# Performance work log

Measured on AMD Instinct MI355X. Metric: run time of the kernel, lower is better.

Reference implementation:

```python
import jax, jax.numpy as jnp
import numpy as np

MARGIN = 0.5
HIERARCHY_LEVEL = 0
EPS = 1e-05


def setup_inputs() -> dict:
    key = jax.random.key(0)
    k1, k2, k3, k4 = jax.random.split(key, 4)
    n, m, d, L, n_classes = 4096, 32768, 128, 2, 100
    embeddings = jax.random.normal(k1, (n, d), dtype=jnp.float32)
    ref_embeddings = jax.random.normal(k2, (m, d), dtype=jnp.float32)
    labels = jax.random.randint(k3, (n, L), 0, n_classes, dtype=jnp.int64)
    ref_labels = jax.random.randint(k4, (m, L), 0, n_classes, dtype=jnp.int64)
    return {"embeddings": embeddings, "labels": labels,
            "ref_embeddings": ref_embeddings, "ref_labels": ref_labels}


def reference(embeddings, labels, ref_embeddings, ref_labels):
    # select hierarchy level
    lab = labels[:, HIERARCHY_LEVEL]          # [n]
    ref_lab = ref_labels[:, HIERARCHY_LEVEL]  # [m]
    n = embeddings.shape[0]
    sim = embeddings @ ref_embeddings.T       # [n, m]
    same = lab[:, None] == ref_lab[None, :]   # [n, m] bool
    # positive pairs: same label and sim < 1 - eps -> contribute (1 - sim)
    pos_mask = same & (sim < 1.0 - EPS)
    # negative pairs: different label and sim > margin -> contribute sim
    neg_mask = (~same) & (sim > MARGIN)
    pos_loss = jnp.sum(jnp.where(pos_mask, 1.0 - sim, 0.0))
    neg_loss = jnp.sum(jnp.where(neg_mask, sim, 0.0))
    return (pos_loss + neg_loss) / n
```

## Files before the change

### kernel.cpp

```cpp
#include <hip/hip_runtime.h>
#include <stdint.h>

#define N_EMB 4096
#define M_REF 32768
#define D_K   128
#define BM    128
#define BN    128
#define NCOLTILES 16
#define COLCHUNK (BN * NCOLTILES)
#define NCCHUNK (M_REF / COLCHUNK)
#define NROWT  (N_EMB / BM)

typedef __attribute__((ext_vector_type(8))) short short8;
typedef __attribute__((ext_vector_type(4))) float float4v;

static __device__ __forceinline__ unsigned short f2bf(float f) {
    unsigned int u = __builtin_bit_cast(unsigned int, f);
    u += 0x7FFFu + ((u >> 16) & 1u);
    return (unsigned short)(u >> 16);
}

__global__ void cvt_kernel(const float* __restrict__ emb, const float* __restrict__ ref,
                           unsigned short* __restrict__ aw, unsigned short* __restrict__ bw) {
    const int NA4 = N_EMB * D_K / 4;
    const int NB4 = M_REF * D_K / 4;
    int stride = gridDim.x * blockDim.x;
    for (int i = blockIdx.x * blockDim.x + threadIdx.x; i < NA4 + NB4; i += stride) {
        const float4* src;
        unsigned short* dst;
        int j;
        if (i < NA4) { src = (const float4*)emb; dst = aw; j = i; }
        else         { src = (const float4*)ref; dst = bw; j = i - NA4; }
        float4 v = src[j];
        ushort4 o;
        o.x = f2bf(v.x); o.y = f2bf(v.y); o.z = f2bf(v.z); o.w = f2bf(v.w);
        *(ushort4*)(dst + (size_t)j * 4) = o;
    }
}

static __device__ __forceinline__ void gld_lds16(const void* g, void* l) {
    __builtin_amdgcn_global_load_lds((__attribute__((address_space(1))) void*)g,
                                     (__attribute__((address_space(3))) void*)l,
                                     16, 0, 0);
}

__launch_bounds__(256, 2)
__global__ void xbm_kernel(const unsigned short* __restrict__ aw,
                           const unsigned short* __restrict__ bw,
                           const int* __restrict__ lab,
                           const int* __restrict__ rlab,
                           float* __restrict__ out) {
    __shared__ unsigned short a_sm[BM * D_K];
    __shared__ unsigned short b_sm[BN * D_K];
    __shared__ float red_sm[4];

    const int tid  = threadIdx.x;
    const int lane = tid & 63;
    const int wave = tid >> 6;
    const int wm = wave >> 1, wn = wave & 1;
    const int quad = lane >> 4;
    const int l15  = lane & 15;

    const int rtile  = blockIdx.x >> 4;
    const int cchunk = blockIdx.x & 15;
    const int row0 = rtile * BM;
    const int col0 = cchunk * COLCHUNK;

    #pragma unroll
    for (int i = 0; i < 8; ++i) {
        int c  = i * 256 + tid;
        int r  = c >> 4;
        int ch = c & 15;
        int sc = ch ^ (r & 15);
        gld_lds16((const char*)aw + ((size_t)(row0 + r) * D_K + sc * 8) * 2,
                  (char*)a_sm + (size_t)c * 16);
    }

    int labv[4][4];
    #pragma unroll
    for (int mt = 0; mt < 4; ++mt)
        #pragma unroll
        for (int r = 0; r < 4; ++r) {
            int row = row0 + wm * 64 + mt * 16 + quad * 4 + r;
            labv[mt][r] = lab[row * 2];
        }

    __syncthreads();

    short8 a_reg[4][4];
    #pragma unroll
    for (int mt = 0; mt < 4; ++mt) {
        int ml = wm * 64 + mt * 16 + l15;
        #pragma unroll
        for (int ks = 0; ks < 4; ++ks) {
            int ch = ks * 4 + quad;
            int cs = ch ^ (ml & 15);
            a_reg[mt][ks] = *(const short8*)(a_sm + (size_t)ml * D_K + cs * 8);
        }
    }

    float loss = 0.0f;

    for (int t = 0; t < NCOLTILES; ++t) {
        const int cbase = col0 + t * BN;

        #pragma unroll
        for (int i = 0; i < 8; ++i) {
            int c  = i * 256 + tid;
            int r  = c >> 4;
            int ch = c & 15;
            int sc = ch ^ (r & 15);
            gld_lds16((const char*)bw + ((size_t)(cbase + r) * D_K + sc * 8) * 2,
                      (char*)b_sm + (size_t)c * 16);
        }
        __syncthreads();

        float4v acc[4][4] = {};
        #pragma unroll
        for (int ks = 0; ks < 4; ++ks) {
            short8 b_reg[4];
            #pragma unroll
            for (int nt = 0; nt < 4; ++nt) {
                int nl = wn * 64 + nt * 16 + l15;
                int ch = ks * 4 + quad;
                int cs = ch ^ (nl & 15);
                b_reg[nt] = *(const short8*)(b_sm + (size_t)nl * D_K + cs * 8);
            }
            #pragma unroll
            for (int mt = 0; mt < 4; ++mt)
                #pragma unroll
                for (int nt = 0; nt < 4; ++nt)
                    acc[mt][nt] = __builtin_amdgcn_mfma_f32_16x16x32_bf16(
                        a_reg[mt][ks], b_reg[nt], acc[mt][nt], 0, 0, 0);
        }
        __syncthreads();

        int rl[4];
        #pragma unroll
        for (int nt = 0; nt < 4; ++nt) {
            int cix = cbase + wn * 64 + nt * 16 + l15;
            rl[nt] = rlab[cix * 2];
        }
        #pragma unroll
        for (int mt = 0; mt < 4; ++mt)
            #pragma unroll
            for (int nt = 0; nt < 4; ++nt)
                #pragma unroll
                for (int r = 0; r < 4; ++r) {
                    float s = acc[mt][nt][r];
                    float pos = fmaxf(1.0f - s, 0.0f);
                    float neg = (s > 0.5f) ? s : 0.0f;
                    loss += (labv[mt][r] == rl[nt]) ? pos : neg;
                }
    }

    #pragma unroll
    for (int off = 32; off > 0; off >>= 1)
        loss += __shfl_down(loss, off, 64);
    if (lane == 0) red_sm[wave] = loss;
    __syncthreads();
    if (tid == 0) {
        float v = (red_sm[0] + red_sm[1] + red_sm[2] + red_sm[3]) * (1.0f / (float)N_EMB);
        atomicAdd(out, v);
    }
}

extern "C" void kernel_launch(void* const* d_in, const int* in_sizes, int n_in,
                              void* d_out, int out_size, void* d_ws, size_t ws_size,
                              hipStream_t stream) {
    const float* emb     = (const float*)d_in[0];
    const int*   labels  = (const int*)d_in[1];
    const float* ref     = (const float*)d_in[2];
    const int*   rlabels = (const int*)d_in[3];
    float* out = (float*)d_out;

    unsigned short* aw = (unsigned short*)d_ws;
    unsigned short* bw = aw + (size_t)N_EMB * D_K;

    hipMemsetAsync(d_out, 0, sizeof(float), stream);
    cvt_kernel<<<512, 256, 0, stream>>>(emb, ref, aw, bw);
    xbm_kernel<<<NROWT * NCCHUNK, 256, 0, stream>>>(aw, bw, labels, rlabels, out);
}
```

Before: 119.0 us.

## Double-buffer B tiles with BN=64, reuse LDS for A, fold memset into convert

Halves the column tile to 64, so the LDS footprint can be reused: the A tile is staged through the two B buffers, then those buffers double-buffer B tiles, prefetching the next tile while MFMAs run on the current one. This removes one barrier per iteration and lets three blocks fit per CU, at the cost of more blocks and more reloads of A per column. The output memset moves into the convert kernel, which now launches twice as many blocks, to save one launch. Loss is accumulated in four partial sums to shorten the dependency chain.

```diff
diff --git a/kernel.cpp b/kernel.cpp
--- a/kernel.cpp
+++ b/kernel.cpp
@@ -5,7 +5,7 @@
 #define M_REF 32768
 #define D_K   128
 #define BM    128
-#define BN    128
+#define BN    64
 #define NCOLTILES 16
 #define COLCHUNK (BN * NCOLTILES)
 #define NCCHUNK (M_REF / COLCHUNK)
@@ -21,7 +21,9 @@
 }
 
 __global__ void cvt_kernel(const float* __restrict__ emb, const float* __restrict__ ref,
-                           unsigned short* __restrict__ aw, unsigned short* __restrict__ bw) {
+                           unsigned short* __restrict__ aw, unsigned short* __restrict__ bw,
+                           float* __restrict__ out) {
+    if (blockIdx.x == 0 && threadIdx.x == 0) out[0] = 0.0f;
     const int NA4 = N_EMB * D_K / 4;
     const int NB4 = M_REF * D_K / 4;
     int stride = gridDim.x * blockDim.x;
@@ -44,14 +46,13 @@
                                      16, 0, 0);
 }
 
-__launch_bounds__(256, 2)
+__launch_bounds__(256, 3)
 __global__ void xbm_kernel(const unsigned short* __restrict__ aw,
                            const unsigned short* __restrict__ bw,
                            const int* __restrict__ lab,
                            const int* __restrict__ rlab,
                            float* __restrict__ out) {
-    __shared__ unsigned short a_sm[BM * D_K];
-    __shared__ unsigned short b_sm[BN * D_K];
+    __shared__ unsigned short sm[2][BN * D_K];
     __shared__ float red_sm[4];
 
     const int tid  = threadIdx.x;
@@ -61,8 +62,8 @@
     const int quad = lane >> 4;
     const int l15  = lane & 15;
 
-    const int rtile  = blockIdx.x >> 4;
-    const int cchunk = blockIdx.x & 15;
+    const int rtile  = blockIdx.x >> 5;
+    const int cchunk = blockIdx.x & 31;
     const int row0 = rtile * BM;
     const int col0 = cchunk * COLCHUNK;
 
@@ -73,7 +74,7 @@
         int ch = c & 15;
         int sc = ch ^ (r & 15);
         gld_lds16((const char*)aw + ((size_t)(row0 + r) * D_K + sc * 8) * 2,
-                  (char*)a_sm + (size_t)c * 16);
+                  (char*)&sm[r >> 6][(r & 63) * D_K + ch * 8]);
     }
 
     int labv[4][4];
@@ -95,64 +96,80 @@
         for (int ks = 0; ks < 4; ++ks) {
             int ch = ks * 4 + quad;
             int cs = ch ^ (ml & 15);
-            a_reg[mt][ks] = *(const short8*)(a_sm + (size_t)ml * D_K + cs * 8);
+            a_reg[mt][ks] = *(const short8*)(&sm[wm][(ml & 63) * D_K + cs * 8]);
         }
     }
 
-    float loss = 0.0f;
+    __syncthreads();
+
+    #pragma unroll
+    for (int i = 0; i < 4; ++i) {
+        int c  = i * 256 + tid;
+        int r  = c >> 4;
+        int ch = c & 15;
+        int sc = ch ^ (r & 15);
+        gld_lds16((const char*)bw + ((size_t)(col0 + r) * D_K + sc * 8) * 2,
+                  (char*)&sm[0][r * D_K + ch * 8]);
+    }
+
+    float lossa[4] = {0.0f, 0.0f, 0.0f, 0.0f};
 
     for (int t = 0; t < NCOLTILES; ++t) {
         const int cbase = col0 + t * BN;
+        const int buf = t & 1;
 
-        #pragma unroll
-        for (int i = 0; i < 8; ++i) {
-            int c  = i * 256 + tid;
-            int r  = c >> 4;
-            int ch = c & 15;
-            int sc = ch ^ (r & 15);
-            gld_lds16((const char*)bw + ((size_t)(cbase + r) * D_K + sc * 8) * 2,
-                      (char*)b_sm + (size_t)c * 16);
-        }
         __syncthreads();
 
-        float4v acc[4][4] = {};
+        if (t + 1 < NCOLTILES) {
+            #pragma unroll
+            for (int i = 0; i < 4; ++i) {
+                int c  = i * 256 + tid;
+                int r  = c >> 4;
+                int ch = c & 15;
+                int sc = ch ^ (r & 15);
+                gld_lds16((const char*)bw + ((size_t)(cbase + BN + r) * D_K + sc * 8) * 2,
+                          (char*)&sm[buf ^ 1][r * D_K + ch * 8]);
+            }
+        }
+
+        int rl[2];
+        #pragma unroll
+        for (int nt = 0; nt < 2; ++nt)
+            rl[nt] = rlab[(cbase + wn * 32 + nt * 16 + l15) * 2];
+
+        float4v acc[4][2] = {};
         #pragma unroll
         for (int ks = 0; ks < 4; ++ks) {
-            short8 b_reg[4];
+            short8 b_reg[2];
             #pragma unroll
-            for (int nt = 0; nt < 4; ++nt) {
-                int nl = wn * 64 + nt * 16 + l15;
+            for (int nt = 0; nt < 2; ++nt) {
+                int nl = wn * 32 + nt * 16 + l15;
                 int ch = ks * 4 + quad;
                 int cs = ch ^ (nl & 15);
-                b_reg[nt] = *(const short8*)(b_sm + (size_t)nl * D_K + cs * 8);
+                b_reg[nt] = *(const short8*)(&sm[buf][nl * D_K + cs * 8]);
             }
             #pragma unroll
             for (int mt = 0; mt < 4; ++mt)
                 #pragma unroll
-                for (int nt = 0; nt < 4; ++nt)
+                for (int nt = 0; nt < 2; ++nt)
                     acc[mt][nt] = __builtin_amdgcn_mfma_f32_16x16x32_bf16(
                         a_reg[mt][ks], b_reg[nt], acc[mt][nt], 0, 0, 0);
         }
-        __syncthreads();
 
-        int rl[4];
-        #pragma unroll
-        for (int nt = 0; nt < 4; ++nt) {
-            int cix = cbase + wn * 64 + nt * 16 + l15;
-            rl[nt] = rlab[cix * 2];
-        }
         #pragma unroll
         for (int mt = 0; mt < 4; ++mt)
             #pragma unroll
-            for (int nt = 0; nt < 4; ++nt)
+            for (int nt = 0; nt < 2; ++nt)
                 #pragma unroll
                 for (int r = 0; r < 4; ++r) {
                     float s = acc[mt][nt][r];
                     float pos = fmaxf(1.0f - s, 0.0f);
                     float neg = (s > 0.5f) ? s : 0.0f;
-                    loss += (labv[mt][r] == rl[nt]) ? pos : neg;
+                    lossa[mt] += (labv[mt][r] == rl[nt]) ? pos : neg;
                 }
     }
+
+    float loss = (lossa[0] + lossa[1]) + (lossa[2] + lossa[3]);
 
     #pragma unroll
     for (int off = 32; off > 0; off >>= 1)
@@ -177,7 +194,6 @@
     unsigned short* aw = (unsigned short*)d_ws;
     unsigned short* bw = aw + (size_t)N_EMB * D_K;
 
-    hipMemsetAsync(d_out, 0, sizeof(float), stream);
-    cvt_kernel<<<512, 256, 0, stream>>>(emb, ref, aw, bw);
+    cvt_kernel<<<1024, 256, 0, stream>>>(emb, ref, aw, bw, out);
     xbm_kernel<<<NROWT * NCCHUNK, 256, 0, stream>>>(aw, bw, labels, rlabels, out);
 }
```

After: 121.5 us. +2.1%, slower.

## Load MFMA operands directly from global, drop LDS staging and memset

Applied to the files above, without the earlier changes.

Removes the LDS staging of A and B tiles and the block barriers; each wave now loads its MFMA fragments straight from global memory, relying on L1/L2 for reuse across waves. The output zeroing moves into the convert kernel in place of a separate memset, the convert grid is doubled, and the loss is split across four accumulators to shorten dependency chains. Without LDS, every wave fetches B through the caches, which raises global traffic and may expose load latency because there is no explicit prefetch.

```diff
diff --git a/kernel.cpp b/kernel.cpp
--- a/kernel.cpp
+++ b/kernel.cpp
@@ -21,7 +21,9 @@
 }
 
 __global__ void cvt_kernel(const float* __restrict__ emb, const float* __restrict__ ref,
-                           unsigned short* __restrict__ aw, unsigned short* __restrict__ bw) {
+                           unsigned short* __restrict__ aw, unsigned short* __restrict__ bw,
+                           float* __restrict__ out) {
+    if (blockIdx.x == 0 && threadIdx.x == 0) out[0] = 0.0f;
     const int NA4 = N_EMB * D_K / 4;
     const int NB4 = M_REF * D_K / 4;
     int stride = gridDim.x * blockDim.x;
@@ -38,20 +40,12 @@
     }
 }
 
-static __device__ __forceinline__ void gld_lds16(const void* g, void* l) {
-    __builtin_amdgcn_global_load_lds((__attribute__((address_space(1))) void*)g,
-                                     (__attribute__((address_space(3))) void*)l,
-                                     16, 0, 0);
-}
-
 __launch_bounds__(256, 2)
 __global__ void xbm_kernel(const unsigned short* __restrict__ aw,
                            const unsigned short* __restrict__ bw,
                            const int* __restrict__ lab,
                            const int* __restrict__ rlab,
                            float* __restrict__ out) {
-    __shared__ unsigned short a_sm[BM * D_K];
-    __shared__ unsigned short b_sm[BN * D_K];
     __shared__ float red_sm[4];
 
     const int tid  = threadIdx.x;
@@ -66,54 +60,32 @@
     const int row0 = rtile * BM;
     const int col0 = cchunk * COLCHUNK;
 
+    short8 a_reg[4][4];
     #pragma unroll
-    for (int i = 0; i < 8; ++i) {
-        int c  = i * 256 + tid;
-        int r  = c >> 4;
-        int ch = c & 15;
-        int sc = ch ^ (r & 15);
-        gld_lds16((const char*)aw + ((size_t)(row0 + r) * D_K + sc * 8) * 2,
-                  (char*)a_sm + (size_t)c * 16);
+    for (int mt = 0; mt < 4; ++mt) {
+        const int row = row0 + wm * 64 + mt * 16 + l15;
+        #pragma unroll
+        for (int ks = 0; ks < 4; ++ks)
+            a_reg[mt][ks] = *(const short8*)(aw + (size_t)row * D_K + ks * 32 + quad * 8);
     }
 
     int labv[4][4];
     #pragma unroll
     for (int mt = 0; mt < 4; ++mt)
         #pragma unroll
-        for (int r = 0; r < 4; ++r) {
-            int row = row0 + wm * 64 + mt * 16 + quad * 4 + r;
-            labv[mt][r] = lab[row * 2];
-        }
+        for (int r = 0; r < 4; ++r)
+            labv[mt][r] = lab[(row0 + wm * 64 + mt * 16 + quad * 4 + r) * 2];
 
-    __syncthreads();
+    float lossa[4] = {0.0f, 0.0f, 0.0f, 0.0f};
 
-    short8 a_reg[4][4];
-    #pragma unroll
-    for (int mt = 0; mt < 4; ++mt) {
-        int ml = wm * 64 + mt * 16 + l15;
-        #pragma unroll
-        for (int ks = 0; ks < 4; ++ks) {
-            int ch = ks * 4 + quad;
-            int cs = ch ^ (ml & 15);
-            a_reg[mt][ks] = *(const short8*)(a_sm + (size_t)ml * D_K + cs * 8);
-        }
-    }
-
-    float loss = 0.0f;
+    const unsigned short* bwt = bw + (size_t)col0 * D_K;
+    const int* rlt = rlab + (size_t)col0 * 2;
 
     for (int t = 0; t < NCOLTILES; ++t) {
-        const int cbase = col0 + t * BN;
-
+        int rl[4];
         #pragma unroll
-        for (int i = 0; i < 8; ++i) {
-            int c  = i * 256 + tid;
-            int r  = c >> 4;
-            int ch = c & 15;
-            int sc = ch ^ (r & 15);
-            gld_lds16((const char*)bw + ((size_t)(cbase + r) * D_K + sc * 8) * 2,
-                      (char*)b_sm + (size_t)c * 16);
-        }
-        __syncthreads();
+        for (int nt = 0; nt < 4; ++nt)
+            rl[nt] = rlt[(wn * 64 + nt * 16 + l15) * 2];
 
         float4v acc[4][4] = {};
         #pragma unroll
@@ -121,10 +93,8 @@
             short8 b_reg[4];
             #pragma unroll
             for (int nt = 0; nt < 4; ++nt) {
-                int nl = wn * 64 + nt * 16 + l15;
-                int ch = ks * 4 + quad;
-                int cs = ch ^ (nl & 15);
-                b_reg[nt] = *(const short8*)(b_sm + (size_t)nl * D_K + cs * 8);
+                const int nl = wn * 64 + nt * 16 + l15;
+                b_reg[nt] = *(const short8*)(bwt + (size_t)nl * D_K + ks * 32 + quad * 8);
             }
             #pragma unroll
             for (int mt = 0; mt < 4; ++mt)
@@ -133,14 +103,7 @@
                     acc[mt][nt] = __builtin_amdgcn_mfma_f32_16x16x32_bf16(
                         a_reg[mt][ks], b_reg[nt], acc[mt][nt], 0, 0, 0);
         }
-        __syncthreads();
 
-        int rl[4];
-        #pragma unroll
-        for (int nt = 0; nt < 4; ++nt) {
-            int cix = cbase + wn * 64 + nt * 16 + l15;
-            rl[nt] = rlab[cix * 2];
-        }
         #pragma unroll
         for (int mt = 0; mt < 4; ++mt)
             #pragma unroll
@@ -150,9 +113,14 @@
                     float s = acc[mt][nt][r];
                     float pos = fmaxf(1.0f - s, 0.0f);
                     float neg = (s > 0.5f) ? s : 0.0f;
-                    loss += (labv[mt][r] == rl[nt]) ? pos : neg;
+                    lossa[mt] += (labv[mt][r] == rl[nt]) ? pos : neg;
                 }
+
+        bwt += (size_t)BN * D_K;
+        rlt += BN * 2;
     }
+
+    float loss = (lossa[0] + lossa[1]) + (lossa[2] + lossa[3]);
 
     #pragma unroll
     for (int off = 32; off > 0; off >>= 1)
@@ -177,7 +145,6 @@
     unsigned short* aw = (unsigned short*)d_ws;
     unsigned short* bw = aw + (size_t)N_EMB * D_K;
 
-    hipMemsetAsync(d_out, 0, sizeof(float), stream);
-    cvt_kernel<<<512, 256, 0, stream>>>(emb, ref, aw, bw);
+    cvt_kernel<<<1024, 256, 0, stream>>>(emb, ref, aw, bw, out);
     xbm_kernel<<<NROWT * NCCHUNK, 256, 0, stream>>>(aw, bw, labels, rlabels, out);
 }
```

After: 152.7 us. 28.4% more time.
